# Performance work log

Measured on AMD Instinct MI355X. Metric: run time of the kernel, lower is better.

Reference implementation:

```python
import jax, jax.numpy as jnp
import numpy as np

N = 30000       # num atoms (all examples concatenated)
E = 480000      # total num edges (avg degree 16)
H = 128         # hidden_channels
R = 50          # num_rbf
NB = 3          # num interaction blocks
NEX = 64        # num examples (molecules)
NTYPES = 100    # atom type vocabulary
CUT = 10.0      # cutoff_upper


def setup_inputs() -> dict:
    key = jax.random.key(0)
    ks = jax.random.split(key, 20)
    s = 0.05
    inp = {
        "pos": jax.random.uniform(ks[0], (N, 3), dtype=jnp.float32) * 10.0,
        "atom_types": jax.random.randint(ks[1], (N,), 0, NTYPES),
        "edge_index": jax.random.randint(ks[2], (2, E), 0, N),
        "batch": jnp.sort(jax.random.randint(ks[3], (N,), 0, NEX)),
        # learned parameters
        "embedding": jax.random.normal(ks[4], (NTYPES, H), dtype=jnp.float32) * s,
        "filt_w1": jax.random.normal(ks[5], (NB, R, H), dtype=jnp.float32) * s,
        "filt_b1": jnp.zeros((NB, H), jnp.float32),
        "filt_w2": jax.random.normal(ks[6], (NB, H, H), dtype=jnp.float32) * s,
        "filt_b2": jnp.zeros((NB, H), jnp.float32),
        "lin1_w": jax.random.normal(ks[7], (NB, H, H), dtype=jnp.float32) * s,  # no bias
        "lin2_w": jax.random.normal(ks[8], (NB, H, H), dtype=jnp.float32) * s,
        "lin2_b": jnp.zeros((NB, H), jnp.float32),
        "blk_w": jax.random.normal(ks[9], (NB, H, H), dtype=jnp.float32) * s,
        "blk_b": jnp.zeros((NB, H), jnp.float32),
        "out_w1": jax.random.normal(ks[10], (H, H // 2), dtype=jnp.float32) * s,
        "out_b1": jnp.zeros((H // 2,), jnp.float32),
        "out_w2": jax.random.normal(ks[11], (H // 2, 1), dtype=jnp.float32) * s,
        "out_b2": jnp.zeros((1,), jnp.float32),
    }
    return inp


def reference(pos, atom_types, edge_index, batch, embedding,
              filt_w1, filt_b1, filt_w2, filt_b2,
              lin1_w, lin2_w, lin2_b, blk_w, blk_b,
              out_w1, out_b1, out_w2, out_b2):
    src, dst = edge_index[0], edge_index[1]
    # pairwise distances along edges
    diff = pos[src] - pos[dst]                        # [E,3]
    d = jnp.sqrt(jnp.sum(diff * diff, axis=-1) + 1e-12)  # [E]
    # Gaussian RBF expansion (PyG GaussianSmearing)
    offset = jnp.linspace(0.0, CUT, R, dtype=jnp.float32)
    coeff = -0.5 / (offset[1] - offset[0]) ** 2
    rbf = jnp.exp(coeff * (d[:, None] - offset) ** 2)  # [E,R]
    # cosine cutoff envelope
    C = 0.5 * (jnp.cos(d * jnp.pi / CUT) + 1.0) * (d < CUT)  # [E]

    x = embedding[atom_types]                         # [N,H]
    for b in range(NB):
        # filter network: Linear -> Tanh -> Linear, modulated by cutoff
        W = jnp.tanh(rbf @ filt_w1[b] + filt_b1[b]) @ filt_w2[b] + filt_b2[b]
        W = W * C[:, None]                            # [E,H]
        # cfconv: lin1 (no bias), gather-multiply-scatter, lin2
        h = x @ lin1_w[b]                             # [N,H]
        msg = h[src] * W                              # [E,H]
        agg = jax.ops.segment_sum(msg, dst, num_segments=N)  # [N,H]
        h = agg @ lin2_w[b] + lin2_b[b]
        # interaction block: activation + linear, residual update
        x = x + (jnp.tanh(h) @ blk_w[b] + blk_b[b])
    # output network: per-atom energy then scatter-sum per molecule
    e = jnp.tanh(x @ out_w1 + out_b1) @ out_w2 + out_b2     # [N,1]
    energy = jax.ops.segment_sum(e, batch, num_segments=NEX)  # [NEX,1]
    return energy.reshape(-1)
```

## Files before the change

kernel.cpp:

```cpp
#include <hip/hip_runtime.h>

typedef unsigned short ushort_t;
typedef _Float16 half8 __attribute__((ext_vector_type(8)));
typedef float f32x4 __attribute__((ext_vector_type(4)));

constexpr int NN  = 30000;
constexpr int EE  = 480000;
constexpr int NEXM = 64;
constexpr int ATB = 16;
constexpr int NSB = (NN + 255) / 256;
constexpr int NBINS = 2048;
constexpr int TROWS = 2064;

#define MFMA16(a,b,c) __builtin_amdgcn_mfma_f32_16x16x32_f16((a),(b),(c),0,0,0)
#define LDS_ADD(p,v) __hip_atomic_fetch_add((p),(v),__ATOMIC_RELAXED,__HIP_MEMORY_SCOPE_WORKGROUP)
#define LGKM_WAIT asm volatile("s_waitcnt lgkmcnt(0)" ::: "memory")

__device__ __forceinline__ float fast_tanh(float x){
  float e2 = __builtin_amdgcn_exp2f(x * 2.885390081777927f);
  return 1.f - 2.f * __builtin_amdgcn_rcpf(e2 + 1.f);
}
__device__ __forceinline__ ushort_t f2h(float v){
  union { _Float16 h; ushort_t s; } cv; cv.h = (_Float16)v; return cv.s;
}

__global__ __launch_bounds__(256) void fused_prep(
  const float* __restrict__ fw1, const float* __restrict__ fb1,
  const float* __restrict__ fw2, const float* __restrict__ l1w,
  const float* __restrict__ l2w, const float* __restrict__ bw,
  const float* __restrict__ ow1, ushort_t* __restrict__ frags,
  const int* __restrict__ ei, int* __restrict__ cnt, float* __restrict__ out)
{
  const int bid = blockIdx.x;
  if (bid < 896){
    if (bid == 0 && threadIdx.x < NEXM) out[threadIdx.x] = 0.f;
    int u = bid*256 + threadIdx.x;
    float val;
    if (u < 24576){
      int b = u >> 13; int v = u & 8191;
      int j = v & 7, lane = (v>>3)&63, fid = v>>9;
      int mt = fid>>1, ks = fid&1;
      int f1 = mt*16 + (lane&15);
      int k  = ks*32 + ((lane>>4)&3)*8 + j;
      val = (k < 50) ? fw1[(b*50 + k)*128 + f1] : (k == 50 ? fb1[b*128 + f1] : 0.f);
    } else if (u < 73728){
      int v = u - 24576; int b = v >> 14; int v2 = v & 16383;
      int j = v2&7, lane = (v2>>3)&63, fid = v2>>9;
      int mt = fid>>2, ks = fid&3;
      int n = mt*16 + (lane&15);
      int k = ks*32 + ((lane>>4)&3)*8 + j;
      val = fw2[b*16384 + k*128 + n];
    } else if (u < 221184){
      int v = u - 73728; int g = v / 49152; int v1 = v - g*49152;
      int b = v1 >> 14; int v2 = v1 & 16383;
      int j = v2&7, lane=(v2>>3)&63, fid=v2>>9;
      int mt = fid>>2, ks = fid&3;
      int n = mt*16 + (lane&15);
      int k = ks*32 + ((lane>>4)&3)*8 + j;
      const float* W = (g==0? l2w : (g==1? bw : l1w));
      val = W[b*16384 + k*128 + n];
    } else {
      int v2 = u - 221184;
      int j = v2&7, lane=(v2>>3)&63, fid=v2>>9;
      int mt = fid>>2, ks = fid&3;
      int n = mt*16 + (lane&15);
      int k = ks*32 + ((lane>>4)&3)*8 + j;
      val = ow1[k*64 + n];
    }
    frags[u] = f2h(val);
  } else {
    int e = (bid-896)*256 + threadIdx.x;
    atomicAdd(cnt + ei[EE + e], 1);
  }
}

__global__ __launch_bounds__(256) void fused_mid(
  const ushort_t* __restrict__ w1a, const ushort_t* __restrict__ w2a,
  const float* __restrict__ fb2, ushort_t* __restrict__ tab,
  const int* __restrict__ cnt, int* __restrict__ seg, int* __restrict__ bsum)
{
  __shared__ ushort_t st[4*2112];
  const int bid = blockIdx.x;
  if (bid < 99){
    const int wave = threadIdx.x>>6, lane = threadIdx.x&63;
    const int quad = lane>>4, n15 = lane&15;
    const int b = bid / 33, tg = bid % 33;
    const int tile = tg*4 + wave;
    if (tile >= TROWS/16) return;
    const half8* w1v = (const half8*)(w1a + b*8192);
    const half8* w2v = (const half8*)(w2a + b*16384);
    ushort_t* tw = st + wave*2112;
    half8 a1[16];
    #pragma unroll
    for (int i=0;i<16;i++) a1[i] = w1v[i*64 + lane];
    f32x4 b2v[8];
    #pragma unroll
    for (int mt=0;mt<8;mt++) b2v[mt] = *(const f32x4*)(fb2 + b*128 + mt*16 + quad*4);
    const f32x4 zero4 = {0.f,0.f,0.f,0.f};
    const float dd = 10.f/49.f;
    const float coefl2 = (-0.5f/(dd*dd)) * 1.4426950408889634f;
    const float dbin = 10.f/(float)NBINS;

    float de = (float)(tile*16 + n15) * dbin;
    float Cv = (de < 10.f) ? 0.5f*(cosf(de*0.31415926535897931f)+1.f) : 0.f;
    half8 rb0, rb1;
    #pragma unroll
    for (int j=0;j<8;j++){
      int k0 = quad*8 + j;
      float t0 = de - (float)k0*dd;
      rb0[j] = (_Float16)__builtin_amdgcn_exp2f(coefl2*t0*t0);
      int k1 = 32 + quad*8 + j;
      float v1;
      if (k1 < 50){ float t1 = de - (float)k1*dd; v1 = __builtin_amdgcn_exp2f(coefl2*t1*t1); }
      else v1 = (k1 == 50) ? 1.f : 0.f;
      rb1[j] = (_Float16)v1;
    }
    f32x4 acc1[8];
    #pragma unroll
    for (int mt=0;mt<8;mt++){
      acc1[mt] = MFMA16(a1[mt*2],   rb0, zero4);
      acc1[mt] = MFMA16(a1[mt*2+1], rb1, acc1[mt]);
    }
    #pragma unroll
    for (int mt=0;mt<8;mt++){
      union { ushort_t s[4]; uint2 v; } pk;
      #pragma unroll
      for (int r=0;r<4;r++) pk.s[r] = f2h(fast_tanh(acc1[mt][r]));
      *(uint2*)(tw + n15*132 + mt*16 + quad*4) = pk.v;
    }
    LGKM_WAIT;
    f32x4 acc2[8];
    #pragma unroll
    for (int mt=0;mt<8;mt++) acc2[mt] = zero4;
    #pragma unroll
    for (int ks=0;ks<4;ks++){
      const ushort_t* ra = tw + n15*132 + ks*32 + quad*8;
      union { uint2 v[2]; half8 h16; } cc;
      cc.v[0] = *(const uint2*)(ra);
      cc.v[1] = *(const uint2*)(ra + 4);
      half8 tb = cc.h16;
      #pragma unroll
      for (int mt=0;mt<8;mt++) acc2[mt] = MFMA16(w2v[(mt*4+ks)*64 + lane], tb, acc2[mt]);
    }
    LGKM_WAIT;
    #pragma unroll
    for (int mt=0;mt<8;mt++){
      f32x4 v = acc2[mt] + b2v[mt];
      union { ushort_t s[4]; uint2 q; } pk;
      #pragma unroll
      for (int r=0;r<4;r++) pk.s[r] = f2h(v[r] * Cv);
      *(uint2*)(tw + n15*132 + mt*16 + quad*4) = pk.q;
    }
    LGKM_WAIT;
    ushort_t* dstb = tab + ((size_t)tile*16)*128 + (size_t)b*TROWS*128;
    #pragma unroll
    for (int it=0;it<4;it++){
      int off = it*512 + lane*8;
      uint4 v = *(const uint4*)(tw + (off>>7)*132 + (off&127));
      *(uint4*)(dstb + (size_t)(off>>7)*128 + (off&127)) = v;
    }
  } else {
    int* ws = (int*)st;
    const int sb = bid - 99;
    int i = sb*256 + threadIdx.x;
    int lane = threadIdx.x & 63, w = threadIdx.x >> 6;
    int v = (i < NN) ? cnt[i] : 0;
    int s = v;
    #pragma unroll
    for (int o=1;o<64;o<<=1){ int t = __shfl_up(s,o,64); if (lane>=o) s += t; }
    if (lane == 63) ws[w] = s;
    __syncthreads();
    int add = 0;
    #pragma unroll
    for (int j=0;j<3;j++) if (w > j) add += ws[j];
    s += add;
    if (i < NN) seg[i] = s - v;
    if (threadIdx.x == 255) bsum[sb] = s;
  }
}

__global__ __launch_bounds__(128) void scan2(int* __restrict__ bsum)
{
  __shared__ int w0tot;
  int tid = threadIdx.x, lane = tid & 63, w = tid >> 6;
  int v = (tid < NSB) ? bsum[tid] : 0;
  int s = v;
  #pragma unroll
  for (int o=1;o<64;o<<=1){ int t = __shfl_up(s,o,64); if (lane>=o) s += t; }
  if (w == 0 && lane == 63) w0tot = s;
  __syncthreads();
  if (w == 1) s += w0tot;
  if (tid < NSB) bsum[tid] = s - v;
}

__global__ __launch_bounds__(256) void scan3(
  int* __restrict__ seg, const int* __restrict__ bsum)
{
  int i = blockIdx.x*256 + threadIdx.x;
  if (i < NN) seg[i] += bsum[blockIdx.x];
}

__global__ __launch_bounds__(256) void fused_tail(
  const float* __restrict__ pos, const int* __restrict__ ei,
  int* __restrict__ off, uint2* __restrict__ meta2,
  const int* __restrict__ atype, const float* __restrict__ emb,
  const ushort_t* __restrict__ l1T, float* __restrict__ x, ushort_t* __restrict__ h)
{
  __shared__ float xbuf[4*2112];
  const int bid = blockIdx.x;
  if (bid < 1875){
    int e = bid*256 + threadIdx.x;
    int s = ei[e], d = ei[EE + e];
    float dx = pos[s*3+0]-pos[d*3+0];
    float dy = pos[s*3+1]-pos[d*3+1];
    float dz = pos[s*3+2]-pos[d*3+2];
    float dist = sqrtf(dx*dx+dy*dy+dz*dz + 1e-12f);
    float t = fminf(dist, 10.f) * ((float)NBINS / 10.f);
    int p = atomicAdd(off + d, 1);
    uint2 m;
    m.x = __float_as_uint(t);
    m.y = (unsigned)s;
    meta2[p] = m;
    return;
  }
  const int vb = bid - 1875;
  const int wave = threadIdx.x>>6, lane = threadIdx.x&63;
  const int quad = lane>>4, n15 = lane&15;
  float* xw = xbuf + wave*2112;
  ushort_t* sw = (ushort_t*)xw;
  const half8* wv = (const half8*)l1T;
  const f32x4 zero4 = {0.f,0.f,0.f,0.f};
  const int ntiles = NN/16;
  const int stride = 512*4;
  for (int tile = vb*4 + wave; tile < ntiles; tile += stride){
    int a0 = tile*16;
    int typ = atype[a0 + n15];
    const f32x4* av = (const f32x4*)(emb + (size_t)typ*128);
    half8 bg[4]; f32x4 xl[4], xh[4];
    #pragma unroll
    for (int ks=0;ks<4;ks++){
      f32x4 lo = av[ks*8 + quad*2];
      f32x4 hi = av[ks*8 + quad*2 + 1];
      xl[ks] = lo; xh[ks] = hi;
      half8 bh;
      #pragma unroll
      for (int i=0;i<4;i++){ bh[i]=(_Float16)lo[i]; bh[4+i]=(_Float16)hi[i]; }
      bg[ks] = bh;
    }
    f32x4 acc[8];
    #pragma unroll
    for (int mt=0;mt<8;mt++) acc[mt] = zero4;
    #pragma unroll
    for (int ks=0;ks<4;ks++){
      #pragma unroll
      for (int mt=0;mt<8;mt++) acc[mt] = MFMA16(wv[(mt*4+ks)*64 + lane], bg[ks], acc[mt]);
    }
    #pragma unroll
    for (int ks=0;ks<4;ks++){
      *(f32x4*)(xw + n15*132 + ks*32 + quad*8)     = xl[ks];
      *(f32x4*)(xw + n15*132 + ks*32 + quad*8 + 4) = xh[ks];
    }
    LGKM_WAIT;
    {
      float* gx = x + (size_t)a0*128;
      #pragma unroll
      for (int it=0;it<8;it++){
        int off2 = it*256 + lane*4;
        f32x4 v = *(const f32x4*)(xw + (off2>>7)*132 + (off2&127));
        *(f32x4*)(gx + off2) = v;
      }
    }
    LGKM_WAIT;
    #pragma unroll
    for (int mt=0;mt<8;mt++){
      union { ushort_t s[4]; uint2 v; } pk;
      #pragma unroll
      for (int r=0;r<4;r++) pk.s[r] = f2h(acc[mt][r]);
      *(uint2*)(sw + n15*132 + mt*16 + quad*4) = pk.v;
    }
    LGKM_WAIT;
    {
      ushort_t* gh = h + (size_t)a0*128;
      #pragma unroll
      for (int it=0;it<4;it++){
        int off2 = it*512 + lane*8;
        uint4 v = *(const uint4*)(sw + (off2>>7)*132 + (off2&127));
        *(uint4*)(gh + off2) = v;
      }
    }
    LGKM_WAIT;
  }
}

__global__ __launch_bounds__(256,8) void mega_pass(
  const uint2* __restrict__ meta2, const ushort_t* __restrict__ hin,
  ushort_t* __restrict__ hout, const ushort_t* __restrict__ tab,
  const ushort_t* __restrict__ l2T, const ushort_t* __restrict__ bkT,
  const ushort_t* __restrict__ l1Tn,
  const float* __restrict__ l2b, const float* __restrict__ bb,
  const int* __restrict__ segend, float* __restrict__ x, int do_h)
{
  __shared__ ushort_t nt[2112];
  const int wave = threadIdx.x>>6, lane = threadIdx.x&63;
  const int quad = lane>>4, n15 = lane&15;
  const int base = blockIdx.x*ATB;
  const f32x4 zero4 = {0.f,0.f,0.f,0.f};

  const int cg = threadIdx.x >> 4, ctf = threadIdx.x & 15;
  const int ca = base + cg;
  const int clo = (ca==0) ? 0 : segend[ca-1];
  const int chi = segend[ca];
  float acc[8];
  #pragma unroll
  for (int j=0;j<8;j++) acc[j] = 0.f;

  if (clo < chi){
    const int last = chi - 1;
    const half8* tabc = (const half8*)tab + ctf;
    const ushort_t* hinc = hin + ctf*8;
    int s0 = clo;
    int cnt = (chi - s0 < 16) ? (chi - s0) : 16;
    int ei0 = s0 + ctf;
    uint2 mm = meta2[(ei0 <= last) ? ei0 : last];
    int ei1 = s0 + 16 + ctf;
    uint2 mq = (s0 + 16 <= last) ? meta2[(ei1 <= last) ? ei1 : last] : mm;
    float fr; half8 w0, w1, hv;
    {
      unsigned mx = __shfl(mm.x, 0, 16);
      unsigned my = __shfl(mm.y, 0, 16);
      float t = __uint_as_float(mx); int i0 = (int)t; fr = t - (float)i0;
      w0 = tabc[(size_t)i0*16];
      w1 = tabc[(size_t)i0*16 + 16];
      hv = *(const half8*)(hinc + (size_t)my*128);
    }
    int j = 0;
    for (;;){
      int jn = j + 1;
      bool more = true;
      if (jn >= cnt){
        if (s0 + 16 > last){ more = false; }
        else {
          s0 += 16;
          cnt = (chi - s0 < 16) ? (chi - s0) : 16;
          mm = mq;
          int ei2 = s0 + 16 + ctf;
          mq = (s0 + 16 <= last) ? meta2[(ei2 <= last) ? ei2 : last] : mm;
          jn = 0;
        }
      }
      float frn = fr; half8 w0n = w0, w1n = w1, hvn = hv;
      if (more){
        unsigned mx = __shfl(mm.x, jn, 16);
        unsigned my = __shfl(mm.y, jn, 16);
        float t = __uint_as_float(mx); int i2 = (int)t; frn = t - (float)i2;
        w0n = tabc[(size_t)i2*16];
        w1n = tabc[(size_t)i2*16 + 16];
        hvn = *(const half8*)(hinc + (size_t)my*128);
      }
      #pragma unroll
      for (int jj=0;jj<8;jj++){
        float wl = (float)w0[jj] + fr * ((float)w1[jj] - (float)w0[jj]);
        acc[jj] += wl * (float)hv[jj];
      }
      if (!more) break;
      w0 = w0n; w1 = w1n; hv = hvn; fr = frn; j = jn;
    }
  }

  {
    union { ushort_t s[8]; uint4 q; } pk;
    #pragma unroll
    for (int j=0;j<8;j++) pk.s[j] = f2h(acc[j]);
    *(uint4*)(nt + cg*132 + ctf*8) = pk.q;
  }
  __syncthreads();

  {
    half8 bg[4];
    #pragma unroll
    for (int ks=0;ks<4;ks++){
      const ushort_t* ra = nt + n15*132 + ks*32 + quad*8;
      union { uint2 v[2]; half8 h16; } cc;
      cc.v[0] = *(const uint2*)(ra);
      cc.v[1] = *(const uint2*)(ra + 4);
      bg[ks] = cc.h16;
    }
    __syncthreads();
    const half8* wAv = (const half8*)l2T;
    f32x4 accA[2];
    #pragma unroll
    for (int i=0;i<2;i++) accA[i] = zero4;
    #pragma unroll
    for (int ks=0;ks<4;ks++){
      #pragma unroll
      for (int i=0;i<2;i++)
        accA[i] = MFMA16(wAv[((wave*2+i)*4+ks)*64 + lane], bg[ks], accA[i]);
    }
    #pragma unroll
    for (int i=0;i<2;i++){
      int mt = wave*2 + i;
      f32x4 bv = *(const f32x4*)(l2b + mt*16 + quad*4);
      union { ushort_t s[4]; uint2 v; } pk;
      #pragma unroll
      for (int r=0;r<4;r++) pk.s[r] = f2h(fast_tanh(accA[i][r] + bv[r]));
      *(uint2*)(nt + n15*132 + mt*16 + quad*4) = pk.v;
    }
    __syncthreads();
    half8 bg2[4];
    #pragma unroll
    for (int ks=0;ks<4;ks++){
      const ushort_t* ra = nt + n15*132 + ks*32 + quad*8;
      union { uint2 v[2]; half8 h16; } cc;
      cc.v[0] = *(const uint2*)(ra);
      cc.v[1] = *(const uint2*)(ra + 4);
      bg2[ks] = cc.h16;
    }
    __syncthreads();
    const half8* wBv = (const half8*)bkT;
    f32x4 accB[2];
    #pragma unroll
    for (int i=0;i<2;i++) accB[i] = zero4;
    #pragma unroll
    for (int ks=0;ks<4;ks++){
      #pragma unroll
      for (int i=0;i<2;i++)
        accB[i] = MFMA16(wBv[((wave*2+i)*4+ks)*64 + lane], bg2[ks], accB[i]);
    }
    f32x4 xn[2];
    float* xp = x + (size_t)(base + n15)*128;
    #pragma unroll
    for (int i=0;i<2;i++){
      int mt = wave*2 + i;
      f32x4 bv = *(const f32x4*)(bb + mt*16 + quad*4);
      f32x4 xv = *(const f32x4*)(xp + mt*16 + quad*4);
      xn[i] = xv + accB[i] + bv;
      *(f32x4*)(xp + mt*16 + quad*4) = xn[i];
    }
    if (do_h){
      #pragma unroll
      for (int i=0;i<2;i++){
        int mt = wave*2 + i;
        union { ushort_t s[4]; uint2 v; } pk;
        #pragma unroll
        for (int r=0;r<4;r++) pk.s[r] = f2h(xn[i][r]);
        *(uint2*)(nt + n15*132 + mt*16 + quad*4) = pk.v;
      }
      __syncthreads();
      half8 bg3[4];
      #pragma unroll
      for (int ks=0;ks<4;ks++){
        const ushort_t* ra = nt + n15*132 + ks*32 + quad*8;
        union { uint2 v[2]; half8 h16; } cc;
        cc.v[0] = *(const uint2*)(ra);
        cc.v[1] = *(const uint2*)(ra + 4);
        bg3[ks] = cc.h16;
      }
      const half8* wCv = (const half8*)l1Tn;
      f32x4 accC[2];
      #pragma unroll
      for (int i=0;i<2;i++) accC[i] = zero4;
      #pragma unroll
      for (int ks=0;ks<4;ks++){
        #pragma unroll
        for (int i=0;i<2;i++)
          accC[i] = MFMA16(wCv[((wave*2+i)*4+ks)*64 + lane], bg3[ks], accC[i]);
      }
      ushort_t* hp = hout + (size_t)(base + n15)*128;
      #pragma unroll
      for (int i=0;i<2;i++){
        int mt = wave*2 + i;
        union { ushort_t s[4]; uint2 v; } pk;
        #pragma unroll
        for (int r=0;r<4;r++) pk.s[r] = f2h(accC[i][r]);
        *(uint2*)(hp + mt*16 + quad*4) = pk.v;
      }
    }
  }
}

__global__ __launch_bounds__(256) void out_head(
  const float* __restrict__ x, const ushort_t* __restrict__ o1T,
  const float* __restrict__ ob1, const float* __restrict__ ow2,
  const float* __restrict__ ob2, const int* __restrict__ batch,
  float* __restrict__ out)
{
  __shared__ float part[NEXM];
  const int tid = threadIdx.x;
  if (tid < NEXM) part[tid] = 0.f;
  __syncthreads();
  const int wave = tid>>6, lane = tid&63;
  const int quad = lane>>4, n15 = lane&15;
  const half8* wv = (const half8*)o1T;
  const f32x4 zero4 = {0.f,0.f,0.f,0.f};
  f32x4 ow2v[4], ob1v[4];
  #pragma unroll
  for (int mt=0;mt<4;mt++){
    ow2v[mt] = *(const f32x4*)(ow2 + mt*16 + quad*4);
    ob1v[mt] = *(const f32x4*)(ob1 + mt*16 + quad*4);
  }
  const float ob2v = ob2[0];
  const int ntiles = NN/16;
  const int stride = gridDim.x*4;
  for (int tile = blockIdx.x*4 + wave; tile < ntiles; tile += stride){
    int a0 = tile*16;
    half8 bg[4];
    const f32x4* av = (const f32x4*)(x + (size_t)(a0 + n15)*128);
    #pragma unroll
    for (int ks=0;ks<4;ks++){
      f32x4 lo = av[ks*8 + quad*2];
      f32x4 hi = av[ks*8 + quad*2 + 1];
      half8 bh;
      #pragma unroll
      for (int i=0;i<4;i++){ bh[i]=(_Float16)lo[i]; bh[4+i]=(_Float16)hi[i]; }
      bg[ks] = bh;
    }
    f32x4 acc[4];
    #pragma unroll
    for (int mt=0;mt<4;mt++) acc[mt] = zero4;
    #pragma unroll
    for (int ks=0;ks<4;ks++){
      #pragma unroll
      for (int mt=0;mt<4;mt++) acc[mt] = MFMA16(wv[(mt*4+ks)*64 + lane], bg[ks], acc[mt]);
    }
    float e = 0.f;
    #pragma unroll
    for (int mt=0;mt<4;mt++){
      f32x4 v = acc[mt] + ob1v[mt];
      #pragma unroll
      for (int r=0;r<4;r++) e += fast_tanh(v[r]) * ow2v[mt][r];
    }
    e += __shfl_xor(e, 16, 64);
    e += __shfl_xor(e, 32, 64);
    if (quad == 0){
      int a = a0 + n15;
      LDS_ADD(&part[batch[a]], e + ob2v);
    }
  }
  __syncthreads();
  if (tid < NEXM)
    __hip_atomic_fetch_add(out + tid, part[tid], __ATOMIC_RELAXED, __HIP_MEMORY_SCOPE_AGENT);
}

extern "C" void kernel_launch(void* const* d_in, const int* in_sizes, int n_in,
                              void* d_out, int out_size, void* d_ws, size_t ws_size,
                              hipStream_t stream)
{
  const float* pos  = (const float*)d_in[0];
  const int*   atyp = (const int*)  d_in[1];
  const int*   ei   = (const int*)  d_in[2];
  const int*   bat  = (const int*)  d_in[3];
  const float* emb  = (const float*)d_in[4];
  const float* fw1  = (const float*)d_in[5];
  const float* fb1  = (const float*)d_in[6];
  const float* fw2  = (const float*)d_in[7];
  const float* fb2  = (const float*)d_in[8];
  const float* l1w  = (const float*)d_in[9];
  const float* l2w  = (const float*)d_in[10];
  const float* l2b  = (const float*)d_in[11];
  const float* bw   = (const float*)d_in[12];
  const float* bb   = (const float*)d_in[13];
  const float* ow1  = (const float*)d_in[14];
  const float* ob1  = (const float*)d_in[15];
  const float* ow2  = (const float*)d_in[16];
  const float* ob2  = (const float*)d_in[17];
  float* out = (float*)d_out;

  char* p = (char*)d_ws;
  uint2*    meta2 = (uint2*)p;   p += (size_t)EE*8;
  ushort_t* hA   = (ushort_t*)p; p += (size_t)NN*128*2;
  ushort_t* hB   = (ushort_t*)p; p += (size_t)NN*128*2;
  float*    x    = (float*)p;    p += (size_t)NN*128*4;
  ushort_t* frags = (ushort_t*)p; p += 229376*2;
  int*      segend = (int*)p;    p += (size_t)NN*4;
  int*      bsum  = (int*)p;     p += 512;
  ushort_t* tab  = (ushort_t*)p; p += (size_t)3*TROWS*128*2;

  int* cnt = (int*)x;

  ushort_t* w1T = frags;
  ushort_t* w2T = frags + 24576;
  ushort_t* l2T = frags + 73728;
  ushort_t* bkT = frags + 122880;
  ushort_t* l1T = frags + 172032;
  ushort_t* o1T = frags + 221184;

  hipMemsetAsync(cnt, 0, NN*sizeof(int), stream);
  fused_prep<<<896+1875,256,0,stream>>>(fw1,fb1,fw2,l1w,l2w,bw,ow1,frags,ei,cnt,out);
  fused_mid<<<99+NSB,256,0,stream>>>(w1T, w2T, fb2, tab, cnt, segend, bsum);
  scan2<<<1,128,0,stream>>>(bsum);
  scan3<<<NSB,256,0,stream>>>(segend, bsum);
  fused_tail<<<1875+512,256,0,stream>>>(pos, ei, segend, meta2,
                                        atyp, emb, l1T, x, hA);

  for (int b=0;b<3;b++){
    const ushort_t* hin = (b & 1) ? hB : hA;
    ushort_t*       hoB = (b & 1) ? hA : hB;
    int do_h = (b < 2) ? 1 : 0;
    mega_pass<<<NN/ATB,256,0,stream>>>(meta2, hin, hoB,
                                       tab + (size_t)b*TROWS*128,
                                       l2T + b*16384, bkT + b*16384,
                                       l1T + ((b<2)?(b+1):0)*16384,
                                       l2b + b*128, bb + b*128,
                                       segend, x, do_h);
  }
  out_head<<<256,256,0,stream>>>(x, o1T, ob1, ow2, ob2, bat, out);
}
```

Baseline: 291.7 us.

## Fold block-sum scan into consumers and process 32 atoms per mega_pass block

Removes the scan3 kernel by adding per-256-atom block offsets directly where segment offsets are consumed (edge scatter in fused_tail and segment bounds in mega_pass). mega_pass now handles two 16-atom tiles per block, halving the grid and amortising weight-fragment loads. This saves one launch but adds extra bsum reads, more LDS, extra barriers and reduced block-level parallelism.

```diff
diff --git a/kernel.cpp b/kernel.cpp
--- a/kernel.cpp
+++ b/kernel.cpp
@@ -7,7 +7,8 @@
 constexpr int NN  = 30000;
 constexpr int EE  = 480000;
 constexpr int NEXM = 64;
-constexpr int ATB = 16;
+constexpr int ATB = 32;
+constexpr int NBLK = (NN + ATB - 1) / ATB;
 constexpr int NSB = (NN + 255) / 256;
 constexpr int NBINS = 2048;
 constexpr int TROWS = 2064;
@@ -193,16 +194,9 @@
   if (tid < NSB) bsum[tid] = s - v;
 }
 
-__global__ __launch_bounds__(256) void scan3(
-  int* __restrict__ seg, const int* __restrict__ bsum)
-{
-  int i = blockIdx.x*256 + threadIdx.x;
-  if (i < NN) seg[i] += bsum[blockIdx.x];
-}
-
 __global__ __launch_bounds__(256) void fused_tail(
   const float* __restrict__ pos, const int* __restrict__ ei,
-  int* __restrict__ off, uint2* __restrict__ meta2,
+  int* __restrict__ seg, const int* __restrict__ bsum, uint2* __restrict__ meta2,
   const int* __restrict__ atype, const float* __restrict__ emb,
   const ushort_t* __restrict__ l1T, float* __restrict__ x, ushort_t* __restrict__ h)
 {
@@ -216,7 +210,7 @@
     float dz = pos[s*3+2]-pos[d*3+2];
     float dist = sqrtf(dx*dx+dy*dy+dz*dz + 1e-12f);
     float t = fminf(dist, 10.f) * ((float)NBINS / 10.f);
-    int p = atomicAdd(off + d, 1);
+    int p = atomicAdd(seg + d, 1) + bsum[d>>8];
     uint2 m;
     m.x = __float_as_uint(t);
     m.y = (unsigned)s;
@@ -298,84 +292,92 @@
   const ushort_t* __restrict__ l2T, const ushort_t* __restrict__ bkT,
   const ushort_t* __restrict__ l1Tn,
   const float* __restrict__ l2b, const float* __restrict__ bb,
-  const int* __restrict__ segend, float* __restrict__ x, int do_h)
+  const int* __restrict__ seg, const int* __restrict__ bsum,
+  float* __restrict__ x, int do_h)
 {
-  __shared__ ushort_t nt[2112];
+  __shared__ ushort_t nt2[2*2112];
   const int wave = threadIdx.x>>6, lane = threadIdx.x&63;
   const int quad = lane>>4, n15 = lane&15;
   const int base = blockIdx.x*ATB;
   const f32x4 zero4 = {0.f,0.f,0.f,0.f};
-
   const int cg = threadIdx.x >> 4, ctf = threadIdx.x & 15;
-  const int ca = base + cg;
-  const int clo = (ca==0) ? 0 : segend[ca-1];
-  const int chi = segend[ca];
-  float acc[8];
-  #pragma unroll
-  for (int j=0;j<8;j++) acc[j] = 0.f;
-
-  if (clo < chi){
-    const int last = chi - 1;
-    const half8* tabc = (const half8*)tab + ctf;
-    const ushort_t* hinc = hin + ctf*8;
-    int s0 = clo;
-    int cnt = (chi - s0 < 16) ? (chi - s0) : 16;
-    int ei0 = s0 + ctf;
-    uint2 mm = meta2[(ei0 <= last) ? ei0 : last];
-    int ei1 = s0 + 16 + ctf;
-    uint2 mq = (s0 + 16 <= last) ? meta2[(ei1 <= last) ? ei1 : last] : mm;
-    float fr; half8 w0, w1, hv;
-    {
-      unsigned mx = __shfl(mm.x, 0, 16);
-      unsigned my = __shfl(mm.y, 0, 16);
-      float t = __uint_as_float(mx); int i0 = (int)t; fr = t - (float)i0;
-      w0 = tabc[(size_t)i0*16];
-      w1 = tabc[(size_t)i0*16 + 16];
-      hv = *(const half8*)(hinc + (size_t)my*128);
-    }
-    int j = 0;
-    for (;;){
-      int jn = j + 1;
-      bool more = true;
-      if (jn >= cnt){
-        if (s0 + 16 > last){ more = false; }
-        else {
-          s0 += 16;
-          cnt = (chi - s0 < 16) ? (chi - s0) : 16;
-          mm = mq;
-          int ei2 = s0 + 16 + ctf;
-          mq = (s0 + 16 <= last) ? meta2[(ei2 <= last) ? ei2 : last] : mm;
-          jn = 0;
+
+  #pragma unroll 1
+  for (int q=0; q<2; ++q){
+    const int ca = base + q*16 + cg;
+    int clo = 0, chi = 0;
+    if (ca < NN){
+      chi = seg[ca] + bsum[ca>>8];
+      clo = (ca==0) ? 0 : (seg[ca-1] + bsum[(ca-1)>>8]);
+    }
+    float acc[8];
+    #pragma unroll
+    for (int j=0;j<8;j++) acc[j] = 0.f;
+
+    if (clo < chi){
+      const int last = chi - 1;
+      const half8* tabc = (const half8*)tab + ctf;
+      const ushort_t* hinc = hin + ctf*8;
+      int s0 = clo;
+      int cnt = (chi - s0 < 16) ? (chi - s0) : 16;
+      int ei0 = s0 + ctf;
+      uint2 mm = meta2[(ei0 <= last) ? ei0 : last];
+      int ei1 = s0 + 16 + ctf;
+      uint2 mq = (s0 + 16 <= last) ? meta2[(ei1 <= last) ? ei1 : last] : mm;
+      float fr; half8 w0, w1, hv;
+      {
+        unsigned mx = __shfl(mm.x, 0, 16);
+        unsigned my = __shfl(mm.y, 0, 16);
+        float t = __uint_as_float(mx); int i0 = (int)t; fr = t - (float)i0;
+        w0 = tabc[(size_t)i0*16];
+        w1 = tabc[(size_t)i0*16 + 16];
+        hv = *(const half8*)(hinc + (size_t)my*128);
+      }
+      int j = 0;
+      for (;;){
+        int jn = j + 1;
+        bool more = true;
+        if (jn >= cnt){
+          if (s0 + 16 > last){ more = false; }
+          else {
+            s0 += 16;
+            cnt = (chi - s0 < 16) ? (chi - s0) : 16;
+            mm = mq;
+            int ei2 = s0 + 16 + ctf;
+            mq = (s0 + 16 <= last) ? meta2[(ei2 <= last) ? ei2 : last] : mm;
+            jn = 0;
+          }
         }
-      }
-      float frn = fr; half8 w0n = w0, w1n = w1, hvn = hv;
-      if (more){
-        unsigned mx = __shfl(mm.x, jn, 16);
-        unsigned my = __shfl(mm.y, jn, 16);
-        float t = __uint_as_float(mx); int i2 = (int)t; frn = t - (float)i2;
-        w0n = tabc[(size_t)i2*16];
-        w1n = tabc[(size_t)i2*16 + 16];
-        hvn = *(const half8*)(hinc + (size_t)my*128);
-      }
-      #pragma unroll
-      for (int jj=0;jj<8;jj++){
-        float wl = (float)w0[jj] + fr * ((float)w1[jj] - (float)w0[jj]);
-        acc[jj] += wl * (float)hv[jj];
-      }
-      if (!more) break;
-      w0 = w0n; w1 = w1n; hv = hvn; fr = frn; j = jn;
-    }
-  }
-
-  {
-    union { ushort_t s[8]; uint4 q; } pk;
+        float frn = fr; half8 w0n = w0, w1n = w1, hvn = hv;
+        if (more){
+          unsigned mx = __shfl(mm.x, jn, 16);
+          unsigned my = __shfl(mm.y, jn, 16);
+          float t = __uint_as_float(mx); int i2 = (int)t; frn = t - (float)i2;
+          w0n = tabc[(size_t)i2*16];
+          w1n = tabc[(size_t)i2*16 + 16];
+          hvn = *(const half8*)(hinc + (size_t)my*128);
+        }
+        #pragma unroll
+        for (int jj=0;jj<8;jj++){
+          float wl = (float)w0[jj] + fr * ((float)w1[jj] - (float)w0[jj]);
+          acc[jj] += wl * (float)hv[jj];
+        }
+        if (!more) break;
+        w0 = w0n; w1 = w1n; hv = hvn; fr = frn; j = jn;
+      }
+    }
+    union { ushort_t s[8]; uint4 qv; } pk;
     #pragma unroll
     for (int j=0;j<8;j++) pk.s[j] = f2h(acc[j]);
-    *(uint4*)(nt + cg*132 + ctf*8) = pk.q;
+    *(uint4*)(nt2 + q*2112 + cg*132 + ctf*8) = pk.qv;
   }
   __syncthreads();
 
-  {
+  #pragma unroll 1
+  for (int t=0; t<2; ++t){
+    ushort_t* nt = nt2 + t*2112;
+    const int baset = base + t*16;
+    const bool vrow = (baset + n15) < NN;
     half8 bg[4];
     #pragma unroll
     for (int ks=0;ks<4;ks++){
@@ -427,14 +429,14 @@
         accB[i] = MFMA16(wBv[((wave*2+i)*4+ks)*64 + lane], bg2[ks], accB[i]);
     }
     f32x4 xn[2];
-    float* xp = x + (size_t)(base + n15)*128;
+    float* xp = x + (size_t)(baset + n15)*128;
     #pragma unroll
     for (int i=0;i<2;i++){
       int mt = wave*2 + i;
       f32x4 bv = *(const f32x4*)(bb + mt*16 + quad*4);
-      f32x4 xv = *(const f32x4*)(xp + mt*16 + quad*4);
+      f32x4 xv = vrow ? *(const f32x4*)(xp + mt*16 + quad*4) : zero4;
       xn[i] = xv + accB[i] + bv;
-      *(f32x4*)(xp + mt*16 + quad*4) = xn[i];
+      if (vrow) *(f32x4*)(xp + mt*16 + quad*4) = xn[i];
     }
     if (do_h){
       #pragma unroll
@@ -465,15 +467,18 @@
         for (int i=0;i<2;i++)
           accC[i] = MFMA16(wCv[((wave*2+i)*4+ks)*64 + lane], bg3[ks], accC[i]);
       }
-      ushort_t* hp = hout + (size_t)(base + n15)*128;
+      ushort_t* hp = hout + (size_t)(baset + n15)*128;
       #pragma unroll
       for (int i=0;i<2;i++){
         int mt = wave*2 + i;
         union { ushort_t s[4]; uint2 v; } pk;
         #pragma unroll
         for (int r=0;r<4;r++) pk.s[r] = f2h(accC[i][r]);
-        *(uint2*)(hp + mt*16 + quad*4) = pk.v;
-      }
+        if (vrow) *(uint2*)(hp + mt*16 + quad*4) = pk.v;
+      }
+      __syncthreads();
+    } else {
+      __syncthreads();
     }
   }
 }
@@ -571,8 +576,8 @@
   ushort_t* hB   = (ushort_t*)p; p += (size_t)NN*128*2;
   float*    x    = (float*)p;    p += (size_t)NN*128*4;
   ushort_t* frags = (ushort_t*)p; p += 229376*2;
-  int*      segend = (int*)p;    p += (size_t)NN*4;
-  int*      bsum  = (int*)p;     p += 512;
+  int*      seg  = (int*)p;      p += (size_t)NN*4;
+  int*      bsum = (int*)p;      p += 512;
   ushort_t* tab  = (ushort_t*)p; p += (size_t)3*TROWS*128*2;
 
   int* cnt = (int*)x;
@@ -586,22 +591,21 @@
 
   hipMemsetAsync(cnt, 0, NN*sizeof(int), stream);
   fused_prep<<<896+1875,256,0,stream>>>(fw1,fb1,fw2,l1w,l2w,bw,ow1,frags,ei,cnt,out);
-  fused_mid<<<99+NSB,256,0,stream>>>(w1T, w2T, fb2, tab, cnt, segend, bsum);
+  fused_mid<<<99+NSB,256,0,stream>>>(w1T, w2T, fb2, tab, cnt, seg, bsum);
   scan2<<<1,128,0,stream>>>(bsum);
-  scan3<<<NSB,256,0,stream>>>(segend, bsum);
-  fused_tail<<<1875+512,256,0,stream>>>(pos, ei, segend, meta2,
+  fused_tail<<<1875+512,256,0,stream>>>(pos, ei, seg, bsum, meta2,
                                         atyp, emb, l1T, x, hA);
 
   for (int b=0;b<3;b++){
     const ushort_t* hin = (b & 1) ? hB : hA;
     ushort_t*       hoB = (b & 1) ? hA : hB;
     int do_h = (b < 2) ? 1 : 0;
-    mega_pass<<<NN/ATB,256,0,stream>>>(meta2, hin, hoB,
-                                       tab + (size_t)b*TROWS*128,
-                                       l2T + b*16384, bkT + b*16384,
-                                       l1T + ((b<2)?(b+1):0)*16384,
-                                       l2b + b*128, bb + b*128,
-                                       segend, x, do_h);
+    mega_pass<<<NBLK,256,0,stream>>>(meta2, hin, hoB,
+                                     tab + (size_t)b*TROWS*128,
+                                     l2T + b*16384, bkT + b*16384,
+                                     l1T + ((b<2)?(b+1):0)*16384,
+                                     l2b + b*128, bb + b*128,
+                                     seg, bsum, x, do_h);
   }
   out_head<<<256,256,0,stream>>>(x, o1T, ob1, ow2, ob2, bat, out);
 }
```

Result: slower. 384.4 us (+31.8%).
